# Kernel optimization log

Hardware: AMD Instinct MI355X
Metric: run time of the kernel (lower is better)

The kernel has to match this reference:

```python
import jax, jax.numpy as jnp
import numpy as np

N_NODES = 50000
N_EDGES = 800000
IN_CH = 256
OUT_CH = 64  # heads=1
NEG_SLOPE = 0.2


def setup_inputs() -> dict:
    key = jax.random.key(0)
    k1, k2, k3, k4, k5 = jax.random.split(key, 5)
    x = jax.random.normal(k1, (N_NODES, IN_CH), dtype=jnp.float32)
    edge_index = jax.random.randint(k2, (2, N_EDGES), 0, N_NODES, dtype=jnp.int64)
    # glorot init for dense weight [out, in] (torch Linear layout) and att [out, 2]
    s_w = np.sqrt(6.0 / (OUT_CH + IN_CH)).astype(np.float32)
    W = jax.random.uniform(k3, (OUT_CH, IN_CH), minval=-s_w, maxval=s_w, dtype=jnp.float32)
    b = jnp.zeros((OUT_CH,), dtype=jnp.float32)
    s_a = np.sqrt(6.0 / (OUT_CH + 2)).astype(np.float32)
    att = jax.random.uniform(k4, (OUT_CH, 2), minval=-s_a, maxval=s_a, dtype=jnp.float32)
    return {"x": x, "edge_index": edge_index, "W": W, "b": b, "att": att}


def reference(x, edge_index, W, b, att):
    n = x.shape[0]
    # dense projection: feature [N, OUT_CH]
    feature = x @ W.T + b
    # per-node attention contributions: e_pre [N, 2]
    e_pre = feature @ att
    tar = edge_index[0]  # flow='target_to_source'
    src = edge_index[1]
    # edge logit = leakyrelu(a_tar(t) + a_src(s)); self-loop logit per node
    logit_edge = jax.nn.leaky_relu(e_pre[tar, 0] + e_pre[src, 1], NEG_SLOPE)
    logit_self = jax.nn.leaky_relu(e_pre[:, 0] + e_pre[:, 1], NEG_SLOPE)
    # segment softmax over {self edge} U {incoming edges} per target node
    m = jnp.maximum(jax.ops.segment_max(logit_edge, tar, num_segments=n), logit_self)
    exp_edge = jnp.exp(logit_edge - m[tar])
    exp_self = jnp.exp(logit_self - m)
    denom = exp_self + jax.ops.segment_sum(exp_edge, tar, num_segments=n)
    alpha = exp_edge / denom[tar]          # [E]
    alpha_self = exp_self / denom          # [N]
    # weighted gather-scatter aggregation (fused_gas_agg)
    msgs = alpha[:, None] * feature[src]   # [E, OUT_CH]
    out = alpha_self[:, None] * feature + jax.ops.segment_sum(msgs, tar, num_segments=n)
    return out
```

## Files before the change

kernel.cpp:

```cpp
#include <hip/hip_runtime.h>
#include <math.h>

#define N_NODES 50000
#define N_EDGES 800000
#define IN_CH 256
#define OUT_CH 64
#define NEG_SLOPE 0.2f

#define SCAN_BLK 256
#define N_SCAN_BLKS ((N_NODES + SCAN_BLK - 1) / SCAN_BLK)

typedef __bf16 bf16x4 __attribute__((ext_vector_type(4)));
typedef __bf16 bf16x8 __attribute__((ext_vector_type(8)));
typedef float  f32x4  __attribute__((ext_vector_type(4)));

__global__ __launch_bounds__(256) void k_gemm(
    const float* __restrict__ x, const float* __restrict__ W,
    const float* __restrict__ bias, const float* __restrict__ att,
    __bf16* __restrict__ featb, float* __restrict__ e0,
    float* __restrict__ e1, int* __restrict__ deg)
{
    __shared__ __bf16 A[64][72];
    __shared__ __bf16 B[64][72];

    const int t    = threadIdx.x;
    const int row0 = blockIdx.x * 64;
    const int wv   = t >> 6;
    const int li   = t & 63;
    const int lm   = li & 15;
    const int lq   = li >> 4;

    if (t < 64 && row0 + t < N_NODES) deg[row0 + t] = 0;

    f32x4 acc[4];
    #pragma unroll
    for (int tn = 0; tn < 4; ++tn) acc[tn] = (f32x4){0.f, 0.f, 0.f, 0.f};

    const int sr = t >> 2;
    const int cq = t & 3;
    const int gr = row0 + sr;
    const bool ok = (gr < N_NODES);

    for (int kc = 0; kc < IN_CH; kc += 64) {
        __syncthreads();
        #pragma unroll
        for (int i = 0; i < 4; ++i) {
            int kk = cq * 16 + i * 4;
            float4 v = make_float4(0.f, 0.f, 0.f, 0.f);
            if (ok)
                v = *reinterpret_cast<const float4*>(&x[(size_t)gr * IN_CH + kc + kk]);
            bf16x4 h = {(__bf16)v.x, (__bf16)v.y, (__bf16)v.z, (__bf16)v.w};
            *reinterpret_cast<bf16x4*>(&A[sr][kk]) = h;

            float4 w1 = *reinterpret_cast<const float4*>(&W[(size_t)sr * IN_CH + kc + kk]);
            bf16x4 g = {(__bf16)w1.x, (__bf16)w1.y, (__bf16)w1.z, (__bf16)w1.w};
            *reinterpret_cast<bf16x4*>(&B[sr][kk]) = g;
        }
        __syncthreads();

        #pragma unroll
        for (int half = 0; half < 2; ++half) {
            int ko = half * 32 + lq * 8;
            bf16x8 a = *reinterpret_cast<const bf16x8*>(&A[wv * 16 + lm][ko]);
            #pragma unroll
            for (int tn = 0; tn < 4; ++tn) {
                bf16x8 b = *reinterpret_cast<const bf16x8*>(&B[tn * 16 + lm][ko]);
                acc[tn] = __builtin_amdgcn_mfma_f32_16x16x32_bf16(a, b, acc[tn], 0, 0, 0);
            }
        }
    }

    float att0[4], att1[4], bv[4];
    #pragma unroll
    for (int tn = 0; tn < 4; ++tn) {
        int c = tn * 16 + lm;
        att0[tn] = att[c * 2 + 0];
        att1[tn] = att[c * 2 + 1];
        bv[tn]   = bias[c];
    }

    float p0[4] = {0.f, 0.f, 0.f, 0.f};
    float p1[4] = {0.f, 0.f, 0.f, 0.f};
    #pragma unroll
    for (int r = 0; r < 4; ++r) {
        int row = row0 + wv * 16 + lq * 4 + r;
        #pragma unroll
        for (int tn = 0; tn < 4; ++tn) {
            float f = acc[tn][r] + bv[tn];
            if (row < N_NODES)
                featb[(size_t)row * OUT_CH + tn * 16 + lm] = (__bf16)f;
            p0[r] += f * att0[tn];
            p1[r] += f * att1[tn];
        }
    }

    #pragma unroll
    for (int m = 1; m < 16; m <<= 1) {
        #pragma unroll
        for (int r = 0; r < 4; ++r) {
            p0[r] += __shfl_xor(p0[r], m, 64);
            p1[r] += __shfl_xor(p1[r], m, 64);
        }
    }
    if (lm == 0) {
        #pragma unroll
        for (int r = 0; r < 4; ++r) {
            int row = row0 + wv * 16 + lq * 4 + r;
            if (row < N_NODES) {
                e0[row] = p0[r];
                e1[row] = p1[r];
            }
        }
    }
}

__global__ __launch_bounds__(256) void k_hist(
    const int* __restrict__ ei, int* __restrict__ deg, int* __restrict__ e_slot)
{
    int e = blockIdx.x * blockDim.x + threadIdx.x;
    if (e >= N_EDGES) return;
    e_slot[e] = atomicAdd(&deg[ei[e]], 1);
}

__global__ __launch_bounds__(SCAN_BLK) void k_scan_blk(
    const int* __restrict__ deg, int* __restrict__ offl, int* __restrict__ bsum)
{
    __shared__ int s[SCAN_BLK];
    int tid = threadIdx.x;
    int i = blockIdx.x * SCAN_BLK + tid;
    int v = (i < N_NODES) ? deg[i] : 0;
    s[tid] = v;
    __syncthreads();
    #pragma unroll
    for (int d = 1; d < SCAN_BLK; d <<= 1) {
        int u = (tid >= d) ? s[tid - d] : 0;
        __syncthreads();
        s[tid] += u;
        __syncthreads();
    }
    if (i < N_NODES) offl[i] = s[tid] - v;
    if (tid == SCAN_BLK - 1) bsum[blockIdx.x] = s[tid];
}

__global__ __launch_bounds__(256) void k_scan_top(
    const int* __restrict__ bsum, int* __restrict__ boff)
{
    __shared__ int s[256];
    int tid = threadIdx.x;
    int v = (tid < N_SCAN_BLKS) ? bsum[tid] : 0;
    s[tid] = v;
    __syncthreads();
    #pragma unroll
    for (int d = 1; d < 256; d <<= 1) {
        int u = (tid >= d) ? s[tid - d] : 0;
        __syncthreads();
        s[tid] += u;
        __syncthreads();
    }
    if (tid < N_SCAN_BLKS) boff[tid] = s[tid] - v;
    if (tid == 0) boff[N_SCAN_BLKS] = N_EDGES;
}

__global__ __launch_bounds__(256) void k_fill(
    const int* __restrict__ ei, const int* __restrict__ offl,
    const int* __restrict__ boff, const int* __restrict__ e_slot,
    int* __restrict__ csr)
{
    int e = blockIdx.x * blockDim.x + threadIdx.x;
    if (e >= N_EDGES) return;
    int tnode = ei[e];
    int snode = ei[N_EDGES + e];
    csr[offl[tnode] + boff[tnode >> 8] + e_slot[e]] = snode;
}

__global__ __launch_bounds__(256) void k_gather(
    const float* __restrict__ e0, const float* __restrict__ e1,
    const __bf16* __restrict__ featb, const int* __restrict__ offl,
    const int* __restrict__ boff, const int* __restrict__ csr,
    float* __restrict__ out)
{
    int t = blockIdx.x * 4 + (threadIdx.x >> 6);
    int c = threadIdx.x & 63;
    if (t >= N_NODES) return;

    float e0t = e0[t];
    float z   = e0t + e1[t];
    float lr  = z > 0.f ? z : NEG_SLOPE * z;
    float wsf = __expf(lr);

    float acc  = wsf * (float)featb[(size_t)t * OUT_CH + c];
    float wsum = wsf;

    int e   = offl[t] + boff[t >> 8];
    int end = (t + 1 < N_NODES) ? (offl[t + 1] + boff[(t + 1) >> 8]) : N_EDGES;

    for (; e + 4 <= end; e += 4) {
        int s0 = csr[e], s1 = csr[e + 1], s2 = csr[e + 2], s3 = csr[e + 3];
        float q0 = e1[s0], q1 = e1[s1], q2 = e1[s2], q3 = e1[s3];
        float f0 = (float)featb[(size_t)s0 * OUT_CH + c];
        float f1 = (float)featb[(size_t)s1 * OUT_CH + c];
        float f2 = (float)featb[(size_t)s2 * OUT_CH + c];
        float f3 = (float)featb[(size_t)s3 * OUT_CH + c];
        float z0 = e0t + q0, z1 = e0t + q1, z2 = e0t + q2, z3 = e0t + q3;
        float w0 = __expf(z0 > 0.f ? z0 : NEG_SLOPE * z0);
        float w1 = __expf(z1 > 0.f ? z1 : NEG_SLOPE * z1);
        float w2 = __expf(z2 > 0.f ? z2 : NEG_SLOPE * z2);
        float w3 = __expf(z3 > 0.f ? z3 : NEG_SLOPE * z3);
        acc += w0 * f0 + w1 * f1 + w2 * f2 + w3 * f3;
        wsum += (w0 + w1) + (w2 + w3);
    }
    for (; e < end; ++e) {
        int s0 = csr[e];
        float q0 = e1[s0];
        float f0 = (float)featb[(size_t)s0 * OUT_CH + c];
        float z0 = e0t + q0;
        float w0 = __expf(z0 > 0.f ? z0 : NEG_SLOPE * z0);
        acc += w0 * f0;
        wsum += w0;
    }
    out[(size_t)t * OUT_CH + c] = acc / wsum;
}

extern "C" void kernel_launch(void* const* d_in, const int* in_sizes, int n_in,
                              void* d_out, int out_size, void* d_ws, size_t ws_size,
                              hipStream_t stream)
{
    const float* x    = (const float*)d_in[0];
    const int*   ei   = (const int*)d_in[1];
    const float* W    = (const float*)d_in[2];
    const float* bias = (const float*)d_in[3];
    const float* att  = (const float*)d_in[4];
    float* out = (float*)d_out;

    __bf16* featb = (__bf16*)d_ws;
    float*  e0    = (float*)(featb + (size_t)N_NODES * OUT_CH);
    float*  e1    = e0 + N_NODES;
    int*    csr   = (int*)(e1 + N_NODES);
    int*    deg   = csr + N_EDGES;
    int*    offl  = deg + N_NODES;
    int*    bsum  = offl + N_NODES;
    int*    boff  = bsum + N_SCAN_BLKS;
    int*    e_slot= boff + N_SCAN_BLKS + 1;

    dim3 blk(256);

    k_gemm<<<dim3((N_NODES + 63) / 64), blk, 0, stream>>>(
        x, W, bias, att, featb, e0, e1, deg);

    k_hist<<<dim3((N_EDGES + 255) / 256), blk, 0, stream>>>(ei, deg, e_slot);

    k_scan_blk<<<dim3(N_SCAN_BLKS), dim3(SCAN_BLK), 0, stream>>>(deg, offl, bsum);
    k_scan_top<<<dim3(1), dim3(256), 0, stream>>>(bsum, boff);

    k_fill<<<dim3((N_EDGES + 255) / 256), blk, 0, stream>>>(
        ei, offl, boff, e_slot, csr);

    k_gather<<<dim3((N_NODES + 3) / 4), blk, 0, stream>>>(
        e0, e1, featb, offl, boff, csr, out);
}
```

Before: 194.0 us.

## Fuse CSR build and gather into one cooperative persistent kernel with 16-bit indices

Replaces the histogram, two scan, fill and gather kernels with a single cooperative kernel. It runs as a grid-stride persistent launch of 1024 blocks and separates the phases with grid.sync(). This is meant to remove several kernel launch gaps and tail effects. CSR neighbour indices and per-edge slots are stored as unsigned short, which cuts memory traffic for the CSR build and gather. In exchange it adds four grid-wide barriers, and it relies on node ids and degrees fitting in 16 bits.

```diff
diff --git a/kernel.cpp b/kernel.cpp
--- a/kernel.cpp
+++ b/kernel.cpp
@@ -1,5 +1,8 @@
 #include <hip/hip_runtime.h>
+#include <hip/hip_cooperative_groups.h>
 #include <math.h>
+
+namespace cg = cooperative_groups;
 
 #define N_NODES 50000
 #define N_EDGES 800000
@@ -9,6 +12,7 @@
 
 #define SCAN_BLK 256
 #define N_SCAN_BLKS ((N_NODES + SCAN_BLK - 1) / SCAN_BLK)
+#define COOP_BLOCKS 1024
 
 typedef __bf16 bf16x4 __attribute__((ext_vector_type(4)));
 typedef __bf16 bf16x8 __attribute__((ext_vector_type(8)));
@@ -114,111 +118,106 @@
     }
 }
 
-__global__ __launch_bounds__(256) void k_hist(
-    const int* __restrict__ ei, int* __restrict__ deg, int* __restrict__ e_slot)
+__global__ __launch_bounds__(256, 4) void k_graph(
+    const int* __restrict__ ei, const float* __restrict__ e0,
+    const float* __restrict__ e1, const __bf16* __restrict__ featb,
+    int* __restrict__ deg, unsigned short* __restrict__ e_slot,
+    int* __restrict__ offl, int* __restrict__ bsum, int* __restrict__ boff,
+    unsigned short* __restrict__ csr, float* __restrict__ out)
 {
-    int e = blockIdx.x * blockDim.x + threadIdx.x;
-    if (e >= N_EDGES) return;
-    e_slot[e] = atomicAdd(&deg[ei[e]], 1);
-}
-
-__global__ __launch_bounds__(SCAN_BLK) void k_scan_blk(
-    const int* __restrict__ deg, int* __restrict__ offl, int* __restrict__ bsum)
-{
-    __shared__ int s[SCAN_BLK];
-    int tid = threadIdx.x;
-    int i = blockIdx.x * SCAN_BLK + tid;
-    int v = (i < N_NODES) ? deg[i] : 0;
-    s[tid] = v;
-    __syncthreads();
-    #pragma unroll
-    for (int d = 1; d < SCAN_BLK; d <<= 1) {
-        int u = (tid >= d) ? s[tid - d] : 0;
-        __syncthreads();
-        s[tid] += u;
-        __syncthreads();
-    }
-    if (i < N_NODES) offl[i] = s[tid] - v;
-    if (tid == SCAN_BLK - 1) bsum[blockIdx.x] = s[tid];
-}
-
-__global__ __launch_bounds__(256) void k_scan_top(
-    const int* __restrict__ bsum, int* __restrict__ boff)
-{
-    __shared__ int s[256];
-    int tid = threadIdx.x;
-    int v = (tid < N_SCAN_BLKS) ? bsum[tid] : 0;
-    s[tid] = v;
-    __syncthreads();
-    #pragma unroll
-    for (int d = 1; d < 256; d <<= 1) {
-        int u = (tid >= d) ? s[tid - d] : 0;
-        __syncthreads();
-        s[tid] += u;
-        __syncthreads();
-    }
-    if (tid < N_SCAN_BLKS) boff[tid] = s[tid] - v;
-    if (tid == 0) boff[N_SCAN_BLKS] = N_EDGES;
-}
-
-__global__ __launch_bounds__(256) void k_fill(
-    const int* __restrict__ ei, const int* __restrict__ offl,
-    const int* __restrict__ boff, const int* __restrict__ e_slot,
-    int* __restrict__ csr)
-{
-    int e = blockIdx.x * blockDim.x + threadIdx.x;
-    if (e >= N_EDGES) return;
-    int tnode = ei[e];
-    int snode = ei[N_EDGES + e];
-    csr[offl[tnode] + boff[tnode >> 8] + e_slot[e]] = snode;
-}
-
-__global__ __launch_bounds__(256) void k_gather(
-    const float* __restrict__ e0, const float* __restrict__ e1,
-    const __bf16* __restrict__ featb, const int* __restrict__ offl,
-    const int* __restrict__ boff, const int* __restrict__ csr,
-    float* __restrict__ out)
-{
-    int t = blockIdx.x * 4 + (threadIdx.x >> 6);
-    int c = threadIdx.x & 63;
-    if (t >= N_NODES) return;
-
-    float e0t = e0[t];
-    float z   = e0t + e1[t];
-    float lr  = z > 0.f ? z : NEG_SLOPE * z;
-    float wsf = __expf(lr);
-
-    float acc  = wsf * (float)featb[(size_t)t * OUT_CH + c];
-    float wsum = wsf;
-
-    int e   = offl[t] + boff[t >> 8];
-    int end = (t + 1 < N_NODES) ? (offl[t + 1] + boff[(t + 1) >> 8]) : N_EDGES;
-
-    for (; e + 4 <= end; e += 4) {
-        int s0 = csr[e], s1 = csr[e + 1], s2 = csr[e + 2], s3 = csr[e + 3];
-        float q0 = e1[s0], q1 = e1[s1], q2 = e1[s2], q3 = e1[s3];
-        float f0 = (float)featb[(size_t)s0 * OUT_CH + c];
-        float f1 = (float)featb[(size_t)s1 * OUT_CH + c];
-        float f2 = (float)featb[(size_t)s2 * OUT_CH + c];
-        float f3 = (float)featb[(size_t)s3 * OUT_CH + c];
-        float z0 = e0t + q0, z1 = e0t + q1, z2 = e0t + q2, z3 = e0t + q3;
-        float w0 = __expf(z0 > 0.f ? z0 : NEG_SLOPE * z0);
-        float w1 = __expf(z1 > 0.f ? z1 : NEG_SLOPE * z1);
-        float w2 = __expf(z2 > 0.f ? z2 : NEG_SLOPE * z2);
-        float w3 = __expf(z3 > 0.f ? z3 : NEG_SLOPE * z3);
-        acc += w0 * f0 + w1 * f1 + w2 * f2 + w3 * f3;
-        wsum += (w0 + w1) + (w2 + w3);
-    }
-    for (; e < end; ++e) {
-        int s0 = csr[e];
-        float q0 = e1[s0];
-        float f0 = (float)featb[(size_t)s0 * OUT_CH + c];
-        float z0 = e0t + q0;
-        float w0 = __expf(z0 > 0.f ? z0 : NEG_SLOPE * z0);
-        acc += w0 * f0;
-        wsum += w0;
-    }
-    out[(size_t)t * OUT_CH + c] = acc / wsum;
+    cg::grid_group grid = cg::this_grid();
+    __shared__ int sh[SCAN_BLK];
+    const int tid  = threadIdx.x;
+    const int gtid = blockIdx.x * 256 + tid;
+    const int nthr = gridDim.x * 256;
+
+    for (int e = gtid; e < N_EDGES; e += nthr)
+        e_slot[e] = (unsigned short)atomicAdd(&deg[ei[e]], 1);
+    grid.sync();
+
+    for (int c = blockIdx.x; c < N_SCAN_BLKS; c += gridDim.x) {
+        int i = c * SCAN_BLK + tid;
+        int v = (i < N_NODES) ? deg[i] : 0;
+        sh[tid] = v;
+        __syncthreads();
+        #pragma unroll
+        for (int d = 1; d < SCAN_BLK; d <<= 1) {
+            int u = (tid >= d) ? sh[tid - d] : 0;
+            __syncthreads();
+            sh[tid] += u;
+            __syncthreads();
+        }
+        if (i < N_NODES) offl[i] = sh[tid] - v;
+        if (tid == SCAN_BLK - 1) bsum[c] = sh[tid];
+        __syncthreads();
+    }
+    grid.sync();
+
+    if (blockIdx.x == 0) {
+        int v = (tid < N_SCAN_BLKS) ? bsum[tid] : 0;
+        sh[tid] = v;
+        __syncthreads();
+        #pragma unroll
+        for (int d = 1; d < 256; d <<= 1) {
+            int u = (tid >= d) ? sh[tid - d] : 0;
+            __syncthreads();
+            sh[tid] += u;
+            __syncthreads();
+        }
+        if (tid < N_SCAN_BLKS) boff[tid] = sh[tid] - v;
+        if (tid == 0) boff[N_SCAN_BLKS] = N_EDGES;
+    }
+    grid.sync();
+
+    for (int e = gtid; e < N_EDGES; e += nthr) {
+        int tnode = ei[e];
+        int snode = ei[N_EDGES + e];
+        csr[offl[tnode] + boff[tnode >> 8] + (int)e_slot[e]] =
+            (unsigned short)snode;
+    }
+    grid.sync();
+
+    const int wid    = gtid >> 6;
+    const int lane   = tid & 63;
+    const int nwaves = gridDim.x << 2;
+    for (int t = wid; t < N_NODES; t += nwaves) {
+        float e0t = e0[t];
+        float z   = e0t + e1[t];
+        float lr  = z > 0.f ? z : NEG_SLOPE * z;
+        float wsf = __expf(lr);
+
+        float acc  = wsf * (float)featb[(size_t)t * OUT_CH + lane];
+        float wsum = wsf;
+
+        int e   = offl[t] + boff[t >> 8];
+        int end = (t + 1 < N_NODES) ? (offl[t + 1] + boff[(t + 1) >> 8]) : N_EDGES;
+
+        for (; e + 4 <= end; e += 4) {
+            int s0 = csr[e], s1 = csr[e + 1], s2 = csr[e + 2], s3 = csr[e + 3];
+            float q0 = e1[s0], q1 = e1[s1], q2 = e1[s2], q3 = e1[s3];
+            float f0 = (float)featb[(size_t)s0 * OUT_CH + lane];
+            float f1 = (float)featb[(size_t)s1 * OUT_CH + lane];
+            float f2 = (float)featb[(size_t)s2 * OUT_CH + lane];
+            float f3 = (float)featb[(size_t)s3 * OUT_CH + lane];
+            float z0 = e0t + q0, z1 = e0t + q1, z2 = e0t + q2, z3 = e0t + q3;
+            float w0 = __expf(z0 > 0.f ? z0 : NEG_SLOPE * z0);
+            float w1 = __expf(z1 > 0.f ? z1 : NEG_SLOPE * z1);
+            float w2 = __expf(z2 > 0.f ? z2 : NEG_SLOPE * z2);
+            float w3 = __expf(z3 > 0.f ? z3 : NEG_SLOPE * z3);
+            acc += w0 * f0 + w1 * f1 + w2 * f2 + w3 * f3;
+            wsum += (w0 + w1) + (w2 + w3);
+        }
+        for (; e < end; ++e) {
+            int s0 = csr[e];
+            float q0 = e1[s0];
+            float f0 = (float)featb[(size_t)s0 * OUT_CH + lane];
+            float z0 = e0t + q0;
+            float w0 = __expf(z0 > 0.f ? z0 : NEG_SLOPE * z0);
+            acc += w0 * f0;
+            wsum += w0;
+        }
+        out[(size_t)t * OUT_CH + lane] = acc / wsum;
+    }
 }
 
 extern "C" void kernel_launch(void* const* d_in, const int* in_sizes, int n_in,
@@ -232,29 +231,24 @@
     const float* att  = (const float*)d_in[4];
     float* out = (float*)d_out;
 
-    __bf16* featb = (__bf16*)d_ws;
-    float*  e0    = (float*)(featb + (size_t)N_NODES * OUT_CH);
-    float*  e1    = e0 + N_NODES;
-    int*    csr   = (int*)(e1 + N_NODES);
-    int*    deg   = csr + N_EDGES;
-    int*    offl  = deg + N_NODES;
-    int*    bsum  = offl + N_NODES;
-    int*    boff  = bsum + N_SCAN_BLKS;
-    int*    e_slot= boff + N_SCAN_BLKS + 1;
-
-    dim3 blk(256);
-
-    k_gemm<<<dim3((N_NODES + 63) / 64), blk, 0, stream>>>(
+    __bf16* featb  = (__bf16*)d_ws;
+    float*  e0     = (float*)(featb + (size_t)N_NODES * OUT_CH);
+    float*  e1     = e0 + N_NODES;
+    int*    deg    = (int*)(e1 + N_NODES);
+    int*    offl   = deg + N_NODES;
+    int*    bsum   = offl + N_NODES;
+    int*    boff   = bsum + N_SCAN_BLKS;
+    unsigned short* csr    = (unsigned short*)(boff + N_SCAN_BLKS + 1);
+    unsigned short* e_slot = csr + N_EDGES;
+
+    k_gemm<<<dim3((N_NODES + 63) / 64), dim3(256), 0, stream>>>(
         x, W, bias, att, featb, e0, e1, deg);
 
-    k_hist<<<dim3((N_EDGES + 255) / 256), blk, 0, stream>>>(ei, deg, e_slot);
-
-    k_scan_blk<<<dim3(N_SCAN_BLKS), dim3(SCAN_BLK), 0, stream>>>(deg, offl, bsum);
-    k_scan_top<<<dim3(1), dim3(256), 0, stream>>>(bsum, boff);
-
-    k_fill<<<dim3((N_EDGES + 255) / 256), blk, 0, stream>>>(
-        ei, offl, boff, e_slot, csr);
-
-    k_gather<<<dim3((N_NODES + 3) / 4), blk, 0, stream>>>(
-        e0, e1, featb, offl, boff, csr, out);
+    void* args[] = {
+        (void*)&ei, (void*)&e0, (void*)&e1, (void*)&featb,
+        (void*)&deg, (void*)&e_slot, (void*)&offl, (void*)&bsum,
+        (void*)&boff, (void*)&csr, (void*)&out
+    };
+    hipLaunchCooperativeKernel((const void*)k_graph, dim3(COOP_BLOCKS),
+                               dim3(256), args, 0, stream);
 }
```

Result: slower. 638.7 us (+229.1%).
